# Kernel optimization log

Hardware: AMD Instinct MI355X
Metric: run time of the kernel (lower is better)

## Reference

```python
import jax, jax.numpy as jnp
import numpy as np

NUM_BANDS = 30
SPLIT_FREQ = 30
M_PARAM = 1
DIM = 2048
BATCH = 16384


def _dct_mat(N):
    # Orthonormal DCT-II matrix D: dct(x) = x @ D.T, idct(y) = y @ D
    n = np.arange(N, dtype=np.float64)
    kk = n[:, None]
    M = np.cos(np.pi * (n + 0.5) * kk / N)
    s = np.full(N, np.sqrt(2.0 / N))
    s[0] = np.sqrt(1.0 / N)
    return jnp.asarray((M * s[:, None]).astype(np.float32))


def _band_scale(freq_weights, k, N):
    # Precompute the per-frequency scale vector the torch loop applies band-by-band.
    pts = np.linspace(0, N - 1, NUM_BANDS + 1).astype(np.int64)  # torch .long() truncation
    scale = jnp.ones((N,), dtype=freq_weights.dtype)
    for i in range(NUM_BANDS):
        s, e = int(pts[i]), int(pts[i + 1])
        if e <= SPLIT_FREQ:
            f = 1.0 + freq_weights[i] * k * (1.0 - i / NUM_BANDS)
        else:
            f = 1.0 - freq_weights[i] * k * (1.0 - (i - NUM_BANDS // M_PARAM) / NUM_BANDS)
        scale = scale.at[s:e].set(f)  # bands are disjoint; base is 1
    return scale


def setup_inputs() -> dict:
    key = jax.random.key(0)
    ks = jax.random.split(key, 6)
    g = 0.02  # small init like xavier_uniform with gain 0.5
    return {
        "x": jax.random.normal(ks[0], (BATCH, DIM), dtype=jnp.float32),
        "freq_weights": jnp.ones((NUM_BANDS,), dtype=jnp.float32),
        "k": jnp.float32(0.3),
        "W1": jax.random.normal(ks[1], (1024, DIM), dtype=jnp.float32) * g,
        "b1": jnp.zeros((1024,), dtype=jnp.float32),
        "W2": jax.random.normal(ks[2], (512, 1024), dtype=jnp.float32) * g,
        "b2": jnp.zeros((512,), dtype=jnp.float32),
        "Wmu": jax.random.normal(ks[3], (256, 512), dtype=jnp.float32) * g,
        "bmu": jnp.zeros((256,), dtype=jnp.float32),
        "Wlv": jax.random.normal(ks[4], (256, 512), dtype=jnp.float32) * g,
        "blv": jnp.zeros((256,), dtype=jnp.float32),
    }


def reference(x, freq_weights, k, W1, b1, W2, b2, Wmu, bmu, Wlv, blv):
    N = x.shape[-1]
    D = _dct_mat(N)
    # DCT -> per-band reweight -> IDCT, fused as two matmuls and one vector multiply
    xd = (x @ D.T) * _band_scale(freq_weights, k, N)
    xe = xd @ D
    h = jax.nn.relu(xe @ W1.T + b1)
    h = jax.nn.relu(h @ W2.T + b2)
    mu = h @ Wmu.T + bmu
    logvar = h @ Wlv.T + blv
    return (mu, logvar)
```

## Files before the change

### kernel.cpp

```cpp
#include <hip/hip_runtime.h>
#include <hip/hip_bf16.h>
#include <math.h>

#define DIM 2048
#define BATCH 16384

typedef __attribute__((ext_vector_type(8))) short short8;
typedef __attribute__((ext_vector_type(4))) short short4v;
typedef __attribute__((ext_vector_type(4))) float floatx4;
typedef unsigned short ushort_t;

__device__ __forceinline__ ushort_t f2bf(float f) {
    union { float f; unsigned u; } v; v.f = f;
    unsigned r = v.u + 0x7FFFu + ((v.u >> 16) & 1u);
    return (ushort_t)(r >> 16);
}

__global__ void k_scale(const float* __restrict__ fw, const float* __restrict__ kp,
                        float* __restrict__ s) {
    int n = blockIdx.x * blockDim.x + threadIdx.x;
    if (n >= DIM) return;
    float kv = kp[0];
    float f = 1.0f;
    for (int i = 0; i < 30; ++i) {
        long s0 = (long)((double)i       * (double)(DIM - 1) / 30.0);
        long e0 = (long)((double)(i + 1) * (double)(DIM - 1) / 30.0);
        if (n >= s0 && n < e0) {
            if (e0 <= 30)
                f = 1.0f + fw[i] * kv * (1.0f - (float)i / 30.0f);
            else
                f = 1.0f - fw[i] * kv * (1.0f - (float)(i - 30) / 30.0f);
        }
    }
    s[n] = f;
}

__global__ void k_gen_d(ushort_t* __restrict__ D, ushort_t* __restrict__ Dt) {
    int idx = blockIdx.x * blockDim.x + threadIdx.x;
    int r = idx >> 11;
    int c = idx & (DIM - 1);
    const float w  = 7.6699039394282058e-4f;
    const float s0 = 0.02209708691207961f;
    const float s1 = 0.03125f;
    int m1 = ((2 * c + 1) * r) & (4 * DIM - 1);
    int m2 = ((2 * r + 1) * c) & (4 * DIM - 1);
    float v1 = __cosf(w * (float)m1) * (r == 0 ? s0 : s1);
    float v2 = __cosf(w * (float)m2) * (c == 0 ? s0 : s1);
    D[idx]  = f2bf(v1);
    Dt[idx] = f2bf(v2);
}

#define U_W1   262144
#define U_W2    65536
#define U_WH    16384
__global__ void k_cast_w(const float* __restrict__ W1, const float* __restrict__ W2,
                         const float* __restrict__ Wmu, const float* __restrict__ Wlv,
                         ushort_t* __restrict__ W1bf, ushort_t* __restrict__ W2bf,
                         ushort_t* __restrict__ Wcat) {
    int i = blockIdx.x * blockDim.x + threadIdx.x;
    const float* src; ushort_t* dst; int u;
    if (i < U_W1)                    { src = W1;  dst = W1bf;             u = i; }
    else if (i < U_W1 + U_W2)        { src = W2;  dst = W2bf;             u = i - U_W1; }
    else if (i < U_W1 + U_W2 + U_WH) { src = Wmu; dst = Wcat;             u = i - U_W1 - U_W2; }
    else                             { src = Wlv; dst = Wcat + 8 * U_WH;  u = i - U_W1 - U_W2 - U_WH; }
    const float4* p = reinterpret_cast<const float4*>(src) + 2 * (size_t)u;
    float4 a = p[0], b = p[1];
    short8 r;
    r[0] = (short)f2bf(a.x); r[1] = (short)f2bf(a.y);
    r[2] = (short)f2bf(a.z); r[3] = (short)f2bf(a.w);
    r[4] = (short)f2bf(b.x); r[5] = (short)f2bf(b.y);
    r[6] = (short)f2bf(b.z); r[7] = (short)f2bf(b.w);
    *reinterpret_cast<short8*>(dst + 8 * (size_t)u) = r;
}

__global__ void k_cast_x(const float* __restrict__ in, ushort_t* __restrict__ out) {
    int i = blockIdx.x * blockDim.x + threadIdx.x;
    const float4* p = reinterpret_cast<const float4*>(in) + 2 * (size_t)i;
    float4 a = p[0], b = p[1];
    short8 r;
    r[0] = (short)f2bf(a.x); r[1] = (short)f2bf(a.y);
    r[2] = (short)f2bf(a.z); r[3] = (short)f2bf(a.w);
    r[4] = (short)f2bf(b.x); r[5] = (short)f2bf(b.y);
    r[6] = (short)f2bf(b.z); r[7] = (short)f2bf(b.w);
    *reinterpret_cast<short8*>(out + 8 * (size_t)i) = r;
}

__global__ void k_red(const float* __restrict__ P, ushort_t* __restrict__ out,
                      const float* __restrict__ scale, int n4, int n4row) {
    int i = blockIdx.x * blockDim.x + threadIdx.x;
    const float4* p = reinterpret_cast<const float4*>(P);
    float4 a = p[i], b = p[i + n4], c = p[i + 2 * n4], d = p[i + 3 * n4];
    float4 s;
    s.x = a.x + b.x + c.x + d.x;
    s.y = a.y + b.y + c.y + d.y;
    s.z = a.z + b.z + c.z + d.z;
    s.w = a.w + b.w + c.w + d.w;
    if (scale) {
        float4 sc = reinterpret_cast<const float4*>(scale)[i & (n4row - 1)];
        s.x *= sc.x; s.y *= sc.y; s.z *= sc.z; s.w *= sc.w;
    }
    short4v o;
    o[0] = (short)f2bf(s.x); o[1] = (short)f2bf(s.y);
    o[2] = (short)f2bf(s.z); o[3] = (short)f2bf(s.w);
    *reinterpret_cast<short4v*>(out + 4 * (size_t)i) = o;
}

template<int TM, int TN, int BK, int EPI, bool SK4>
__device__ __forceinline__ void gemm_core(
        const ushort_t* __restrict__ A, const ushort_t* __restrict__ B,
        ushort_t* __restrict__ Cb, float* __restrict__ Cf,
        const float* __restrict__ ep0, const float* __restrict__ ep1,
        int M, int N, int K, int KC) {
    constexpr int BM = 32 * TM;
    constexpr int BN = 32 * TN;
    constexpr int SEGS = BK / 8;
    constexpr int RSH  = (BK == 32) ? 1 : 0;
    constexpr int SSH  = (SEGS == 4) ? 2 : 3;
    __shared__ __align__(16) ushort_t As[BM * BK];
    __shared__ __align__(16) ushort_t Bs[BN * BK];

    const int tid  = threadIdx.x;
    const int lane = tid & 63;
    const int wave = tid >> 6;
    const int wm   = wave >> 1;
    const int wn   = wave & 1;
    const int q    = lane >> 4;
    const int l16  = lane & 15;

    const int tilesM = M / BM;
    const int tilesN = N / BN;
    int bid = (int)blockIdx.x;
    int sk = 0;
    if constexpr (SK4) { int nt = tilesM * tilesN; sk = bid / nt; bid = bid % nt; }
    const int xcd = bid & 7;
    const int j   = bid >> 3;
    const int bm  = xcd * (tilesM >> 3) + j / tilesN;
    const int bn  = j % tilesN;

    floatx4 acc[TM][TN];
    #pragma unroll
    for (int i = 0; i < TM; ++i)
        #pragma unroll
        for (int jj = 0; jj < TN; ++jj)
            acc[i][jj] = (floatx4){0.f, 0.f, 0.f, 0.f};

    const long aBase = (long)bm * BM * K + (long)sk * KC;
    const long bBase = (long)bn * BN * K + (long)sk * KC;
    const int  KLOOP = SK4 ? KC : K;

    for (int kt = 0; kt < KLOOP; kt += BK) {
        __syncthreads();
        #pragma unroll
        for (int i = 0; i < BM * BK / 2048; ++i) {
            int idx = tid + i * 256;
            int row = idx >> SSH, seg = idx & (SEGS - 1);
            int gseg = seg ^ ((row >> RSH) & (SEGS - 1));
            const ushort_t* g = A + aBase + (long)row * K + kt + gseg * 8;
            __builtin_amdgcn_global_load_lds(
                (const __attribute__((address_space(1))) void*)g,
                (__attribute__((address_space(3))) void*)(As + idx * 8),
                16, 0, 0);
        }
        #pragma unroll
        for (int i = 0; i < BN * BK / 2048; ++i) {
            int idx = tid + i * 256;
            int row = idx >> SSH, seg = idx & (SEGS - 1);
            int gseg = seg ^ ((row >> RSH) & (SEGS - 1));
            const ushort_t* g = B + bBase + (long)row * K + kt + gseg * 8;
            __builtin_amdgcn_global_load_lds(
                (const __attribute__((address_space(1))) void*)g,
                (__attribute__((address_space(3))) void*)(Bs + idx * 8),
                16, 0, 0);
        }
        __syncthreads();

        #pragma unroll
        for (int ks = 0; ks < BK / 32; ++ks) {
            short8 af[TM], bfr[TN];
            #pragma unroll
            for (int t = 0; t < TM; ++t) {
                int srow = wm * TM * 16 + t * 16 + l16;
                int rseg = (ks * 4 + q) ^ ((srow >> RSH) & (SEGS - 1));
                af[t] = *reinterpret_cast<const short8*>(&As[srow * BK + rseg * 8]);
            }
            #pragma unroll
            for (int t = 0; t < TN; ++t) {
                int srow = wn * TN * 16 + t * 16 + l16;
                int rseg = (ks * 4 + q) ^ ((srow >> RSH) & (SEGS - 1));
                bfr[t] = *reinterpret_cast<const short8*>(&Bs[srow * BK + rseg * 8]);
            }
            #pragma unroll
            for (int i = 0; i < TM; ++i)
                #pragma unroll
                for (int jj = 0; jj < TN; ++jj)
                    acc[i][jj] = __builtin_amdgcn_mfma_f32_16x16x32_bf16(
                        af[i], bfr[jj], acc[i][jj], 0, 0, 0);
        }
    }

    #pragma unroll
    for (int i = 0; i < TM; ++i) {
        #pragma unroll
        for (int jj = 0; jj < TN; ++jj) {
            #pragma unroll
            for (int r = 0; r < 4; ++r) {
                int row = bm * BM + wm * TM * 16 + i * 16 + q * 4 + r;
                int col = bn * BN + wn * TN * 16 + jj * 16 + l16;
                float v = acc[i][jj][r];
                if constexpr (EPI == 0) {
                    Cb[(long)row * N + col] = f2bf(v * ep0[col]);
                } else if constexpr (EPI == 1) {
                    Cb[(long)row * N + col] = f2bf(v);
                } else if constexpr (EPI == 2) {
                    v += ep0[col];
                    v = v > 0.f ? v : 0.f;
                    Cb[(long)row * N + col] = f2bf(v);
                } else if constexpr (EPI == 3) {
                    const int half = N >> 1;
                    if (col < half)
                        Cf[(long)row * half + col] = v + ep0[col];
                    else
                        Cf[(long)M * half + (long)row * half + (col - half)] = v + ep1[col - half];
                } else {
                    Cf[(long)sk * M * N + (long)row * N + col] = v;
                }
            }
        }
    }
}

__global__ __launch_bounds__(512, 2) void g2_256(const ushort_t* __restrict__ A,
        const ushort_t* __restrict__ B, ushort_t* __restrict__ Cb,
        const float* __restrict__ bias, int M, int N, int K) {
    constexpr int BM = 256, BN = 256, BK = 32;
    __shared__ __align__(16) ushort_t As[4][BM * BK];
    __shared__ __align__(16) ushort_t Bs[4][BN * BK];

    const int tid  = threadIdx.x;
    const int lane = tid & 63;
    const int wave = tid >> 6;
    const int wm   = wave >> 2;
    const int wn   = wave & 3;
    const int q    = lane >> 4;
    const int l16  = lane & 15;

    const int tilesM = M / BM;
    const int tilesN = N / BN;
    int bid = (int)blockIdx.x;
    const int xcd = bid & 7;
    const int jb  = bid >> 3;
    const int bm  = xcd * (tilesM >> 3) + jb / tilesN;
    const int bn  = jb % tilesN;
    const int NT  = K / BK;

    const long aBase = (long)bm * BM * K;
    const long bBase = (long)bn * BN * K;

    floatx4 acc[8][4];
    #pragma unroll
    for (int i = 0; i < 8; ++i)
        #pragma unroll
        for (int j = 0; j < 4; ++j)
            acc[i][j] = (floatx4){0.f, 0.f, 0.f, 0.f};

#define STAGE_A(t) do { int _sl = (t) & 3;                                          \
        _Pragma("unroll")                                                           \
        for (int _g = 0; _g < 2; ++_g) {                                            \
            int _idx = _g * 512 + tid;                                              \
            int _row = _idx >> 2, _seg = _idx & 3;                                  \
            int _gs = _seg ^ ((_row >> 1) & 3);                                     \
            const ushort_t* _gp = A + aBase + (long)_row * K + (t) * BK + _gs * 8;  \
            __builtin_amdgcn_global_load_lds(                                       \
                (const __attribute__((address_space(1))) void*)_gp,                 \
                (__attribute__((address_space(3))) void*)(&As[_sl][_idx * 8]),      \
                16, 0, 0);                                                          \
        } } while (0)
#define STAGE_B(t) do { int _sl = (t) & 3;                                          \
        _Pragma("unroll")                                                           \
        for (int _g = 0; _g < 2; ++_g) {                                            \
            int _idx = _g * 512 + tid;                                              \
            int _row = _idx >> 2, _seg = _idx & 3;                                  \
            int _gs = _seg ^ ((_row >> 1) & 3);                                     \
            const ushort_t* _gp = B + bBase + (long)_row * K + (t) * BK + _gs * 8;  \
            __builtin_amdgcn_global_load_lds(                                       \
                (const __attribute__((address_space(1))) void*)_gp,                 \
                (__attribute__((address_space(3))) void*)(&Bs[_sl][_idx * 8]),      \
                16, 0, 0);                                                          \
        } } while (0)

    STAGE_A(0); STAGE_B(0);
    STAGE_A(1); STAGE_B(1);
    STAGE_A(2); STAGE_B(2);
    asm volatile("s_waitcnt vmcnt(8)" ::: "memory");
    __builtin_amdgcn_s_barrier();
    asm volatile("" ::: "memory");

#define KTILE(tt, DOSTAGE, WAITOP) do {                                             \
        const int _slot = (tt) & 3;                                                 \
        short8 bfrag[4], afrag[4];                                                  \
        _Pragma("unroll")                                                           \
        for (int _j = 0; _j < 4; ++_j) {                                            \
            int _sr = wn * 64 + _j * 16 + l16;                                      \
            int _rs = q ^ ((_sr >> 1) & 3);                                         \
            bfrag[_j] = *reinterpret_cast<const short8*>(&Bs[_slot][_sr * BK + _rs * 8]); \
        }                                                                           \
        _Pragma("unroll")                                                           \
        for (int _i = 0; _i < 4; ++_i) {                                            \
            int _sr = wm * 128 + _i * 16 + l16;                                     \
            int _rs = q ^ ((_sr >> 1) & 3);                                         \
            afrag[_i] = *reinterpret_cast<const short8*>(&As[_slot][_sr * BK + _rs * 8]); \
        }                                                                           \
        if (DOSTAGE) STAGE_A((tt) + 3);                                             \
        __builtin_amdgcn_s_barrier();                                               \
        asm volatile("s_waitcnt lgkmcnt(0)" ::: "memory");                          \
        __builtin_amdgcn_sched_barrier(0);                                          \
        __builtin_amdgcn_s_setprio(1);                                              \
        _Pragma("unroll")                                                           \
        for (int _i = 0; _i < 4; ++_i)                                              \
            _Pragma("unroll")                                                       \
            for (int _j = 0; _j < 4; ++_j)                                          \
                acc[_i][_j] = __builtin_amdgcn_mfma_f32_16x16x32_bf16(              \
                    afrag[_i], bfrag[_j], acc[_i][_j], 0, 0, 0);                    \
        __builtin_amdgcn_s_setprio(0);                                              \
        __builtin_amdgcn_s_barrier();                                               \
        asm volatile("" ::: "memory");                                              \
        short8 afrag2[4];                                                           \
        _Pragma("unroll")                                                           \
        for (int _i = 0; _i < 4; ++_i) {                                            \
            int _sr = wm * 128 + 64 + _i * 16 + l16;                                \
            int _rs = q ^ ((_sr >> 1) & 3);                                         \
            afrag2[_i] = *reinterpret_cast<const short8*>(&As[_slot][_sr * BK + _rs * 8]); \
        }                                                                           \
        if (DOSTAGE) STAGE_B((tt) + 3);                                             \
        __builtin_amdgcn_s_barrier();                                               \
        asm volatile("s_waitcnt lgkmcnt(0)" ::: "memory");                          \
        __builtin_amdgcn_sched_barrier(0);                                          \
        __builtin_amdgcn_s_setprio(1);                                              \
        _Pragma("unroll")                                                           \
        for (int _i = 0; _i < 4; ++_i)                                              \
            _Pragma("unroll")                                                       \
            for (int _j = 0; _j < 4; ++_j)                                          \
                acc[4 + _i][_j] = __builtin_amdgcn_mfma_f32_16x16x32_bf16(          \
                    afrag2[_i], bfrag[_j], acc[4 + _i][_j], 0, 0, 0);               \
        __builtin_amdgcn_s_setprio(0);                                              \
        WAITOP;                                                                     \
        __builtin_amdgcn_s_barrier();                                               \
        asm volatile("" ::: "memory");                                              \
    } while (0)

    int t = 0;
    for (; t < NT - 3; ++t) {
        KTILE(t, true, asm volatile("s_waitcnt vmcnt(8)" ::: "memory"));
    }
    KTILE(t, false, asm volatile("s_waitcnt vmcnt(4)" ::: "memory")); ++t;
    KTILE(t, false, asm volatile("s_waitcnt vmcnt(0)" ::: "memory")); ++t;
    KTILE(t, false, (void)0);

#undef KTILE
#undef STAGE_A
#undef STAGE_B

    float bsv[4];
    #pragma unroll
    for (int j = 0; j < 4; ++j)
        bsv[j] = bias[bn * BN + wn * 64 + j * 16 + l16];
    #pragma unroll
    for (int i = 0; i < 8; ++i) {
        int row = bm * BM + wm * 128 + i * 16 + q * 4;
        #pragma unroll
        for (int j = 0; j < 4; ++j) {
            int col = bn * BN + wn * 64 + j * 16 + l16;
            #pragma unroll
            for (int r = 0; r < 4; ++r) {
                float v = acc[i][j][r] + bsv[j];
                v = v > 0.f ? v : 0.f;
                Cb[(long)(row + r) * N + col] = f2bf(v);
            }
        }
    }
}

__global__ __launch_bounds__(256) void g0p_sk(const ushort_t* A, const ushort_t* B,
        float* P, int M, int N, int K, int KC) {
    gemm_core<4, 4, 32, 4, true>(A, B, nullptr, P, nullptr, nullptr, M, N, K, KC);
}
__global__ __launch_bounds__(256) void g1p_sk(const ushort_t* A, const ushort_t* B,
        float* P, int M, int N, int K, int KC) {
    gemm_core<4, 4, 32, 4, true>(A, B, nullptr, P, nullptr, nullptr, M, N, K, KC);
}
__global__ __launch_bounds__(256) void g3_h2(const ushort_t* A, const ushort_t* B,
        ushort_t* Cb, const float* ep0, int M, int N, int K) {
    gemm_core<4, 4, 32, 2, false>(A, B, Cb, nullptr, ep0, nullptr, M, N, K, 0);
}
__global__ __launch_bounds__(256) void g4_head(const ushort_t* A, const ushort_t* B,
        float* Cf, const float* ep0, const float* ep1, int M, int N, int K) {
    gemm_core<4, 4, 32, 3, false>(A, B, nullptr, Cf, ep0, ep1, M, N, K, 0);
}

extern "C" void kernel_launch(void* const* d_in, const int* in_sizes, int n_in,
                              void* d_out, int out_size, void* d_ws, size_t ws_size,
                              hipStream_t stream) {
    const float* x   = (const float*)d_in[0];
    const float* fw  = (const float*)d_in[1];
    const float* kp  = (const float*)d_in[2];
    const float* W1  = (const float*)d_in[3];
    const float* b1  = (const float*)d_in[4];
    const float* W2  = (const float*)d_in[5];
    const float* b2  = (const float*)d_in[6];
    const float* Wmu = (const float*)d_in[7];
    const float* bmu = (const float*)d_in[8];
    const float* Wlv = (const float*)d_in[9];
    const float* blv = (const float*)d_in[10];
    float* out = (float*)d_out;

    char* ws = (char*)d_ws;
    const size_t MB = 1024 * 1024;
    ushort_t* W1bf = (ushort_t*)(ws + 0);
    ushort_t* Dbf  = (ushort_t*)(ws + 4   * MB);
    ushort_t* Dtbf = (ushort_t*)(ws + 12  * MB);
    ushort_t* T1sT = (ushort_t*)(ws + 20  * MB);
    ushort_t* H1   = (ushort_t*)(ws + 0);
    float*    P    = (float*)   (ws + 32  * MB);
    ushort_t* Xbf  = (ushort_t*)(ws + 32  * MB);
    ushort_t* H2   = (ushort_t*)(ws + 96  * MB);
    ushort_t* M1T  = (ushort_t*)(ws + 112 * MB);
    ushort_t* W2bf = (ushort_t*)(ws + 116 * MB);
    ushort_t* Wcat = (ushort_t*)(ws + 117 * MB);
    float*    svec = (float*)   (ws + 118 * MB);

    hipLaunchKernelGGL(k_scale, dim3(DIM / 256), dim3(256), 0, stream, fw, kp, svec);
    hipLaunchKernelGGL(k_gen_d, dim3(DIM * DIM / 256), dim3(256), 0, stream, Dbf, Dtbf);
    hipLaunchKernelGGL(k_cast_w, dim3((U_W1 + U_W2 + 2 * U_WH) / 256), dim3(256), 0, stream,
                       W1, W2, Wmu, Wlv, W1bf, W2bf, Wcat);

    hipLaunchKernelGGL(g0p_sk, dim3(8 * 16 * 4), dim3(256), 0, stream,
                       W1bf, Dbf, P, 1024, 2048, 2048, 512);
    hipLaunchKernelGGL(k_red, dim3(1024 * 2048 / 4 / 256), dim3(256), 0, stream,
                       P, T1sT, svec, 1024 * 2048 / 4, 2048 / 4);
    hipLaunchKernelGGL(g1p_sk, dim3(8 * 16 * 4), dim3(256), 0, stream,
                       T1sT, Dtbf, P, 1024, 2048, 2048, 512);
    hipLaunchKernelGGL(k_red, dim3(1024 * 2048 / 4 / 256), dim3(256), 0, stream,
                       P, M1T, nullptr, 1024 * 2048 / 4, 2048 / 4);

    hipLaunchKernelGGL(k_cast_x, dim3(BATCH * DIM / 8 / 256), dim3(256), 0, stream, x, Xbf);

    hipLaunchKernelGGL(g2_256, dim3((BATCH / 256) * (1024 / 256)), dim3(512), 0, stream,
                       Xbf, M1T, H1, b1, BATCH, 1024, 2048);
    hipLaunchKernelGGL(g3_h2, dim3((BATCH / 128) * (512 / 128)), dim3(256), 0, stream,
                       H1, W2bf, H2, b2, BATCH, 512, 1024);
    hipLaunchKernelGGL(g4_head, dim3((BATCH / 128) * (512 / 128)), dim3(256), 0, stream,
                       H2, Wcat, out, bmu, blv, BATCH, 512, 512);

    (void)in_sizes; (void)n_in; (void)out_size; (void)ws_size;
}
```

Before: 397.0 us.

## Merge K-tile halves in g2_256 and add pipelined 128x128 GEMM for later layers

The g2_256 K-tile loop now loads all A and B fragments up front, issues both next-stage global loads together, and runs all 32 MFMAs between a single pair of barrier points instead of two half-phases with four barriers. A new 128x128 global_load_lds kernel with a four-slot pipeline and XCD-aware tile mapping replaces the generic gemm_core for the W2 layer and the mu/logvar head, with launch bounds of two blocks per CU. Fewer barriers and deeper prefetch aim to cut synchronisation stalls. Holding more fragments live raises register pressure, and there is less interleaving of LDS reads with MFMAs.

```diff
diff --git a/kernel.cpp b/kernel.cpp
--- a/kernel.cpp
+++ b/kernel.cpp
@@ -207,11 +207,7 @@
                 int row = bm * BM + wm * TM * 16 + i * 16 + q * 4 + r;
                 int col = bn * BN + wn * TN * 16 + jj * 16 + l16;
                 float v = acc[i][jj][r];
-                if constexpr (EPI == 0) {
-                    Cb[(long)row * N + col] = f2bf(v * ep0[col]);
-                } else if constexpr (EPI == 1) {
-                    Cb[(long)row * N + col] = f2bf(v);
-                } else if constexpr (EPI == 2) {
+                if constexpr (EPI == 2) {
                     v += ep0[col];
                     v = v > 0.f ? v : 0.f;
                     Cb[(long)row * N + col] = f2bf(v);
@@ -229,6 +225,7 @@
     }
 }
 
+
 __global__ __launch_bounds__(512, 2) void g2_256(const ushort_t* __restrict__ A,
         const ushort_t* __restrict__ B, ushort_t* __restrict__ Cb,
         const float* __restrict__ bias, int M, int N, int K) {
@@ -297,52 +294,42 @@
 
 #define KTILE(tt, DOSTAGE, WAITOP) do {                                             \
         const int _slot = (tt) & 3;                                                 \
-        short8 bfrag[4], afrag[4];                                                  \
+        short8 _bf[4], _alo[4], _ahi[4];                                            \
         _Pragma("unroll")                                                           \
         for (int _j = 0; _j < 4; ++_j) {                                            \
             int _sr = wn * 64 + _j * 16 + l16;                                      \
             int _rs = q ^ ((_sr >> 1) & 3);                                         \
-            bfrag[_j] = *reinterpret_cast<const short8*>(&Bs[_slot][_sr * BK + _rs * 8]); \
+            _bf[_j] = *reinterpret_cast<const short8*>(&Bs[_slot][_sr * BK + _rs * 8]); \
         }                                                                           \
         _Pragma("unroll")                                                           \
         for (int _i = 0; _i < 4; ++_i) {                                            \
             int _sr = wm * 128 + _i * 16 + l16;                                     \
             int _rs = q ^ ((_sr >> 1) & 3);                                         \
-            afrag[_i] = *reinterpret_cast<const short8*>(&As[_slot][_sr * BK + _rs * 8]); \
+            _alo[_i] = *reinterpret_cast<const short8*>(&As[_slot][_sr * BK + _rs * 8]); \
         }                                                                           \
-        if (DOSTAGE) STAGE_A((tt) + 3);                                             \
-        __builtin_amdgcn_s_barrier();                                               \
-        asm volatile("s_waitcnt lgkmcnt(0)" ::: "memory");                          \
-        __builtin_amdgcn_sched_barrier(0);                                          \
+        _Pragma("unroll")                                                           \
+        for (int _i = 0; _i < 4; ++_i) {                                            \
+            int _sr = wm * 128 + 64 + _i * 16 + l16;                                \
+            int _rs = q ^ ((_sr >> 1) & 3);                                         \
+            _ahi[_i] = *reinterpret_cast<const short8*>(&As[_slot][_sr * BK + _rs * 8]); \
+        }                                                                           \
+        if (DOSTAGE) { STAGE_A((tt) + 3); STAGE_B((tt) + 3); }                      \
         __builtin_amdgcn_s_setprio(1);                                              \
         _Pragma("unroll")                                                           \
         for (int _i = 0; _i < 4; ++_i)                                              \
             _Pragma("unroll")                                                       \
             for (int _j = 0; _j < 4; ++_j)                                          \
                 acc[_i][_j] = __builtin_amdgcn_mfma_f32_16x16x32_bf16(              \
-                    afrag[_i], bfrag[_j], acc[_i][_j], 0, 0, 0);                    \
-        __builtin_amdgcn_s_setprio(0);                                              \
-        __builtin_amdgcn_s_barrier();                                               \
-        asm volatile("" ::: "memory");                                              \
-        short8 afrag2[4];                                                           \
-        _Pragma("unroll")                                                           \
-        for (int _i = 0; _i < 4; ++_i) {                                            \
-            int _sr = wm * 128 + 64 + _i * 16 + l16;                                \
-            int _rs = q ^ ((_sr >> 1) & 3);                                         \
-            afrag2[_i] = *reinterpret_cast<const short8*>(&As[_slot][_sr * BK + _rs * 8]); \
-        }                                                                           \
-        if (DOSTAGE) STAGE_B((tt) + 3);                                             \
-        __builtin_amdgcn_s_barrier();                                               \
-        asm volatile("s_waitcnt lgkmcnt(0)" ::: "memory");                          \
-        __builtin_amdgcn_sched_barrier(0);                                          \
-        __builtin_amdgcn_s_setprio(1);                                              \
+                    _alo[_i], _bf[_j], acc[_i][_j], 0, 0, 0);                       \
         _Pragma("unroll")                                                           \
         for (int _i = 0; _i < 4; ++_i)                                              \
             _Pragma("unroll")                                                       \
             for (int _j = 0; _j < 4; ++_j)                                          \
                 acc[4 + _i][_j] = __builtin_amdgcn_mfma_f32_16x16x32_bf16(          \
-                    afrag2[_i], bfrag[_j], acc[4 + _i][_j], 0, 0, 0);               \
+                    _ahi[_i], _bf[_j], acc[4 + _i][_j], 0, 0, 0);                   \
         __builtin_amdgcn_s_setprio(0);                                              \
+        asm volatile("s_waitcnt lgkmcnt(0)" ::: "memory");                          \
+        __builtin_amdgcn_sched_barrier(0);                                          \
         WAITOP;                                                                     \
         __builtin_amdgcn_s_barrier();                                               \
         asm volatile("" ::: "memory");                                              \
@@ -380,6 +367,144 @@
     }
 }
 
+template<int EPI>
+__device__ __forceinline__ void gemm128_v2(
+        const ushort_t* __restrict__ A, const ushort_t* __restrict__ B,
+        ushort_t* __restrict__ Cb, float* __restrict__ Cf,
+        const float* __restrict__ ep0, const float* __restrict__ ep1,
+        int M, int N, int K) {
+    constexpr int BM = 128, BN = 128, BK = 32;
+    __shared__ __align__(16) ushort_t As[4][BM * BK];
+    __shared__ __align__(16) ushort_t Bs[4][BN * BK];
+
+    const int tid  = threadIdx.x;
+    const int lane = tid & 63;
+    const int wave = tid >> 6;
+    const int wm   = wave >> 1;
+    const int wn   = wave & 1;
+    const int q    = lane >> 4;
+    const int l16  = lane & 15;
+
+    const int tilesM = M / BM;
+    const int tilesN = N / BN;
+    int bid = (int)blockIdx.x;
+    const int xcd = bid & 7;
+    const int jb  = bid >> 3;
+    const int bm  = xcd * (tilesM >> 3) + jb / tilesN;
+    const int bn  = jb % tilesN;
+    const int NT  = K / BK;
+
+    const long aBase = (long)bm * BM * K;
+    const long bBase = (long)bn * BN * K;
+
+    floatx4 acc[4][4];
+    #pragma unroll
+    for (int i = 0; i < 4; ++i)
+        #pragma unroll
+        for (int j = 0; j < 4; ++j)
+            acc[i][j] = (floatx4){0.f, 0.f, 0.f, 0.f};
+
+#define STAGE_A(t) do { int _sl = (t) & 3;                                          \
+        _Pragma("unroll")                                                           \
+        for (int _g = 0; _g < 2; ++_g) {                                            \
+            int _idx = _g * 256 + tid;                                              \
+            int _row = _idx >> 2, _seg = _idx & 3;                                  \
+            int _gs = _seg ^ ((_row >> 1) & 3);                                     \
+            const ushort_t* _gp = A + aBase + (long)_row * K + (t) * BK + _gs * 8;  \
+            __builtin_amdgcn_global_load_lds(                                       \
+                (const __attribute__((address_space(1))) void*)_gp,                 \
+                (__attribute__((address_space(3))) void*)(&As[_sl][_idx * 8]),      \
+                16, 0, 0);                                                          \
+        } } while (0)
+#define STAGE_B(t) do { int _sl = (t) & 3;                                          \
+        _Pragma("unroll")                                                           \
+        for (int _g = 0; _g < 2; ++_g) {                                            \
+            int _idx = _g * 256 + tid;                                              \
+            int _row = _idx >> 2, _seg = _idx & 3;                                  \
+            int _gs = _seg ^ ((_row >> 1) & 3);                                     \
+            const ushort_t* _gp = B + bBase + (long)_row * K + (t) * BK + _gs * 8;  \
+            __builtin_amdgcn_global_load_lds(                                       \
+                (const __attribute__((address_space(1))) void*)_gp,                 \
+                (__attribute__((address_space(3))) void*)(&Bs[_sl][_idx * 8]),      \
+                16, 0, 0);                                                          \
+        } } while (0)
+
+    STAGE_A(0); STAGE_B(0);
+    STAGE_A(1); STAGE_B(1);
+    STAGE_A(2); STAGE_B(2);
+    asm volatile("s_waitcnt vmcnt(8)" ::: "memory");
+    __builtin_amdgcn_s_barrier();
+    asm volatile("" ::: "memory");
+
+#define KTILE(tt, DOSTAGE, WAITOP) do {                                             \
+        const int _slot = (tt) & 3;                                                 \
+        short8 _bf[4], _af[4];                                                      \
+        _Pragma("unroll")                                                           \
+        for (int _j = 0; _j < 4; ++_j) {                                            \
+            int _sr = wn * 64 + _j * 16 + l16;                                      \
+            int _rs = q ^ ((_sr >> 1) & 3);                                         \
+            _bf[_j] = *reinterpret_cast<const short8*>(&Bs[_slot][_sr * BK + _rs * 8]); \
+        }                                                                           \
+        _Pragma("unroll")                                                           \
+        for (int _i = 0; _i < 4; ++_i) {                                            \
+            int _sr = wm * 64 + _i * 16 + l16;                                      \
+            int _rs = q ^ ((_sr >> 1) & 3);                                         \
+            _af[_i] = *reinterpret_cast<const short8*>(&As[_slot][_sr * BK + _rs * 8]); \
+        }                                                                           \
+        if (DOSTAGE) { STAGE_A((tt) + 3); STAGE_B((tt) + 3); }                      \
+        __builtin_amdgcn_s_setprio(1);                                              \
+        _Pragma("unroll")                                                           \
+        for (int _i = 0; _i < 4; ++_i)                                              \
+            _Pragma("unroll")                                                       \
+            for (int _j = 0; _j < 4; ++_j)                                          \
+                acc[_i][_j] = __builtin_amdgcn_mfma_f32_16x16x32_bf16(              \
+                    _af[_i], _bf[_j], acc[_i][_j], 0, 0, 0);                        \
+        __builtin_amdgcn_s_setprio(0);                                              \
+        asm volatile("s_waitcnt lgkmcnt(0)" ::: "memory");                          \
+        __builtin_amdgcn_sched_barrier(0);                                          \
+        WAITOP;                                                                     \
+        __builtin_amdgcn_s_barrier();                                               \
+        asm volatile("" ::: "memory");                                              \
+    } while (0)
+
+    int t = 0;
+    for (; t < NT - 3; ++t) {
+        KTILE(t, true, asm volatile("s_waitcnt vmcnt(8)" ::: "memory"));
+    }
+    KTILE(t, false, asm volatile("s_waitcnt vmcnt(4)" ::: "memory")); ++t;
+    KTILE(t, false, asm volatile("s_waitcnt vmcnt(0)" ::: "memory")); ++t;
+    KTILE(t, false, (void)0);
+
+#undef KTILE
+#undef STAGE_A
+#undef STAGE_B
+
+    #pragma unroll
+    for (int i = 0; i < 4; ++i) {
+        #pragma unroll
+        for (int jj = 0; jj < 4; ++jj) {
+            #pragma unroll
+            for (int r = 0; r < 4; ++r) {
+                int row = bm * BM + wm * 64 + i * 16 + q * 4 + r;
+                int col = bn * BN + wn * 64 + jj * 16 + l16;
+                float v = acc[i][jj][r];
+                if constexpr (EPI == 2) {
+                    v += ep0[col];
+                    v = v > 0.f ? v : 0.f;
+                    Cb[(long)row * N + col] = f2bf(v);
+                } else {
+                    const int half = N >> 1;
+                    v += (col < half) ? ep0[col] : ep1[col - half];
+                    if (col < half)
+                        Cf[(long)row * half + col] = v;
+                    else
+                        Cf[(long)M * half + (long)row * half + (col - half)] = v;
+                }
+            }
+        }
+    }
+}
+
 __global__ __launch_bounds__(256) void g0p_sk(const ushort_t* A, const ushort_t* B,
         float* P, int M, int N, int K, int KC) {
     gemm_core<4, 4, 32, 4, true>(A, B, nullptr, P, nullptr, nullptr, M, N, K, KC);
@@ -388,13 +513,13 @@
         float* P, int M, int N, int K, int KC) {
     gemm_core<4, 4, 32, 4, true>(A, B, nullptr, P, nullptr, nullptr, M, N, K, KC);
 }
-__global__ __launch_bounds__(256) void g3_h2(const ushort_t* A, const ushort_t* B,
+__global__ __launch_bounds__(256, 2) void g3_h2(const ushort_t* A, const ushort_t* B,
         ushort_t* Cb, const float* ep0, int M, int N, int K) {
-    gemm_core<4, 4, 32, 2, false>(A, B, Cb, nullptr, ep0, nullptr, M, N, K, 0);
-}
-__global__ __launch_bounds__(256) void g4_head(const ushort_t* A, const ushort_t* B,
+    gemm128_v2<2>(A, B, Cb, nullptr, ep0, nullptr, M, N, K);
+}
+__global__ __launch_bounds__(256, 2) void g4_head(const ushort_t* A, const ushort_t* B,
         float* Cf, const float* ep0, const float* ep1, int M, int N, int K) {
-    gemm_core<4, 4, 32, 3, false>(A, B, nullptr, Cf, ep0, ep1, M, N, K, 0);
+    gemm128_v2<3>(A, B, nullptr, Cf, ep0, ep1, M, N, K);
 }
 
 extern "C" void kernel_launch(void* const* d_in, const int* in_sizes, int n_in,
```

After: 377.3 us. -5.0%, faster.
